# Performance work log

Hardware: AMD Instinct MI355X
Metric: run time of the kernel (lower is better)

Reference implementation:

```python
import jax, jax.numpy as jnp
import numpy as np

WINDOW_SIZE = 11
WINDOW_SIGMA = 1.5
LOSS_WEIGHT = 1.0
PAD = WINDOW_SIZE // 2  # 5; applied to BOTH H and W as in the torch source


def _gaussian_window(channels):
    # Matches torch gaussian_window: 1-D gaussian reshaped to (1,1,1,ws),
    # repeated per channel -> OIHW kernel of shape (C, 1, 1, ws).
    coords = np.arange(WINDOW_SIZE, dtype=np.float32) - (WINDOW_SIZE // 2)
    g = np.exp(-coords ** 2 / (2.0 * WINDOW_SIGMA ** 2))
    g = g / g.sum()
    w = np.tile(g.reshape(1, 1, 1, WINDOW_SIZE), (channels, 1, 1, 1))
    return jnp.asarray(w)


def _dwconv(x, w, channels):
    # Depthwise conv, kernel (1, ws), zero padding 5 on both H and W
    # (faithful to F.conv2d(..., padding=5) with a (1,11) kernel, which
    # grows H by 10 -- intentional reproduction of the source behavior).
    return jax.lax.conv_general_dilated(
        x, w,
        window_strides=(1, 1),
        padding=((PAD, PAD), (PAD, PAD)),
        dimension_numbers=('NCHW', 'OIHW', 'NCHW'),
        feature_group_count=channels,
    )


def setup_inputs() -> dict:
    key = jax.random.key(0)
    k1, k2 = jax.random.split(key)
    shape = (16, 3, 512, 512)
    pred = jax.random.uniform(k1, shape, dtype=jnp.float32)
    target = jax.random.uniform(k2, shape, dtype=jnp.float32)
    return {"pred": pred, "target": target}


def reference(pred, target):
    channels = pred.shape[1]
    w = _gaussian_window(channels)
    conv = lambda x: _dwconv(x, w, channels)

    mu1 = conv(pred)              # (B, C, H+10, W)
    mu2 = conv(target)
    mu1_sq = mu1 * mu1
    mu2_sq = mu2 * mu2
    mu1_mu2 = mu1 * mu2

    sigma1_sq = conv(pred * pred) - mu1_sq
    sigma2_sq = conv(target * target) - mu2_sq
    sigma12 = conv(pred * target) - mu1_mu2

    C1 = 0.01 ** 2
    C2 = 0.03 ** 2
    ssim_map = ((2.0 * mu1_mu2 + C1) * (2.0 * sigma12 + C2)) / (
        (mu1_sq + mu2_sq + C1) * (sigma1_sq + sigma2_sq + C2))

    return LOSS_WEIGHT * (1.0 - ssim_map.mean())
```

## Files before the change

kernel.cpp:

```cpp
#include <hip/hip_runtime.h>
#include <hip/hip_fp16.h>
#include <cmath>

#define WS 11

typedef unsigned int u32x4_t __attribute__((ext_vector_type(4)));

struct GaussHalf {
    unsigned gA[WS];
    unsigned gS[WS];
    unsigned c11, c22;
};

__device__ __forceinline__ u32x4_t make_row_srsrc(const float* p) {
    const unsigned long long a = (unsigned long long)p;
    u32x4_t r;
    r.x = (unsigned)a;
    r.y = (unsigned)(a >> 32);
    r.z = 2048u;
    r.w = 0x00020000u;
    return r;
}
__device__ __forceinline__ float4 bl_x4(u32x4_t srd, int voff) {
    float4 d;
    asm volatile("buffer_load_dwordx4 %0, %1, %2, 0 offen"
                 : "=v"(d) : "v"(voff), "s"(srd));
    return d;
}
__device__ __forceinline__ float bl_x1(u32x4_t srd, int voff) {
    float d;
    asm volatile("buffer_load_dword %0, %1, %2, 0 offen"
                 : "=v"(d) : "v"(voff), "s"(srd));
    return d;
}

__global__ __launch_bounds__(128, 6) void ssim_row_kernel(
    const float* __restrict__ pred, const float* __restrict__ targ,
    GaussHalf gh, float* __restrict__ partials)
{
    const int t = threadIdx.x;
    const int lane = t & 63;
    const int wid = __builtin_amdgcn_readfirstlane((blockIdx.x << 1) | (t >> 6));

    const int l8 = 8 * lane;
    const int vL1 = 4 * (l8 - 5);
    const int vL4 = 4 * (l8 - 4);
    const int vA  = 4 * l8;
    const int vB  = 4 * (l8 + 4);
    const int vR4 = 4 * (l8 + 8);
    const int vR1 = 4 * (l8 + 12);

    const u32x4_t sp = make_row_srsrc(pred + (long long)wid * 512);
    const u32x4_t sq = make_row_srsrc(targ + (long long)wid * 512);

    const float  pL1 = bl_x1(sp, vL1);
    const float4 pL4 = bl_x4(sp, vL4);
    const float4 pA  = bl_x4(sp, vA);
    const float4 pB  = bl_x4(sp, vB);
    const float4 pR4 = bl_x4(sp, vR4);
    const float  pR1 = bl_x1(sp, vR1);
    const float  qL1 = bl_x1(sq, vL1);
    const float4 qL4 = bl_x4(sq, vL4);
    const float4 qA  = bl_x4(sq, vA);
    const float4 qB  = bl_x4(sq, vB);
    const float4 qR4 = bl_x4(sq, vR4);
    const float  qR1 = bl_x1(sq, vR1);
    asm volatile("s_waitcnt vmcnt(0)" ::: "memory");
    __builtin_amdgcn_sched_barrier(0);

    const float pv[18] = {pL1, pL4.x, pL4.y, pL4.z, pL4.w,
                          pA.x, pA.y, pA.z, pA.w, pB.x, pB.y, pB.z, pB.w,
                          pR4.x, pR4.y, pR4.z, pR4.w, pR1};
    const float qv[18] = {qL1, qL4.x, qL4.y, qL4.z, qL4.w,
                          qA.x, qA.y, qA.z, qA.w, qB.x, qB.y, qB.z, qB.w,
                          qR4.x, qR4.y, qR4.z, qR4.w, qR1};

    const __half2 pm = __halves2half2(__float2half(1.f), __float2half(-1.f));
    const __half2 C11 = __builtin_bit_cast(__half2, gh.c11);
    const __half2 C22 = __builtin_bit_cast(__half2, gh.c22);

    __half2 w[18], s[18];
    #pragma unroll
    for (int i = 0; i < 18; ++i) {
        w[i] = __floats2half2_rn(pv[i] + qv[i], pv[i] - qv[i]);
        s[i] = __hmul2(w[i], w[i]);
    }

    float acc = 0.f;
    #pragma unroll
    for (int px = 0; px < 8; ++px) {
        __half2 AB  = __builtin_bit_cast(__half2, 0u);
        __half2 SUV = __builtin_bit_cast(__half2, 0u);
        #pragma unroll
        for (int k = 0; k < WS; ++k) {
            AB  = __hfma2(__builtin_bit_cast(__half2, gh.gA[k]),
                          w[px + k], AB);
            SUV = __hfma2(__builtin_bit_cast(__half2, gh.gS[k]),
                          s[px + k], SUV);
        }
        const __half2 ab2  = __hmul2(AB, AB);
        const __half2 t2d2 = __hfma2(__lowhigh2highlow(ab2), pm, ab2);
        const __half2 tsds = __hfma2(__lowhigh2highlow(SUV), pm, SUV);
        const __half2 dn1  = __hfma2(t2d2, pm, C11);
        const __half2 dl   = __hsub2(tsds, t2d2);
        const __half2 dn2  = __hfma2(dl, pm, C22);
        const __half2 nd   = __hmul2(dn1, dn2);
        const float dd = __half2float(__low2half(nd));
        const float nn = __half2float(__high2half(nd));
        acc = fmaf(nn, __builtin_amdgcn_rcpf(dd), acc);
    }

    #pragma unroll
    for (int offr = 32; offr > 0; offr >>= 1)
        acc += __shfl_down(acc, offr);
    if (lane == 0)
        partials[wid] = acc;
}

__global__ __launch_bounds__(1024) void ssim_final_kernel(
    const float* __restrict__ partials, float* __restrict__ out)
{
    const int t = threadIdx.x;
    double d = 0.0;
    #pragma unroll
    for (int i = 0; i < 24; ++i)
        d += (double)partials[t + 1024 * i];
    #pragma unroll
    for (int offr = 32; offr > 0; offr >>= 1)
        d += __shfl_down(d, offr);
    __shared__ double wsumd[16];
    const int lane = t & 63, wave = t >> 6;
    if (lane == 0) wsumd[wave] = d;
    __syncthreads();
    if (t == 0) {
        double s = 245760.0;
        #pragma unroll
        for (int i = 0; i < 16; ++i) s += wsumd[i];
        out[0] = (float)(1.0 - s / 12828672.0);
    }
}

static unsigned packh2(float x) {
    const __half h = __float2half(x);
    unsigned short hb;
    __builtin_memcpy(&hb, &h, 2);
    return ((unsigned)hb << 16) | hb;
}

extern "C" void kernel_launch(void* const* d_in, const int* in_sizes, int n_in,
                              void* d_out, int out_size, void* d_ws, size_t ws_size,
                              hipStream_t stream) {
    const float* pred = (const float*)d_in[0];
    const float* targ = (const float*)d_in[1];
    float* out = (float*)d_out;
    float* partials = (float*)d_ws;

    GaussHalf gh;
    double graw[WS], s = 0.0;
    for (int i = 0; i < WS; ++i) {
        const double c = (double)(i - WS / 2);
        graw[i] = exp(-c * c / (2.0 * 1.5 * 1.5));
        s += graw[i];
    }
    for (int i = 0; i < WS; ++i) {
        const double g = graw[i] / s;
        gh.gA[i] = packh2((float)(g * 0.70710678118654752));
        gh.gS[i] = packh2((float)(g * 0.5));
    }
    gh.c11 = packh2(0.0001f);
    gh.c22 = packh2(0.0009f);

    ssim_row_kernel<<<12288, 128, 0, stream>>>(pred, targ, gh, partials);
    ssim_final_kernel<<<1, 1024, 0, stream>>>(partials, out);
}
```

Baseline: 26.58 us.

## Process six rows per wave with software-pipelined buffer loads

Each wave now handles six consecutive rows instead of one. Loads for the next row are issued before the current row is computed, with partial vmcnt waits, so memory latency overlaps the half-precision arithmetic. The grid shrinks to 1024 blocks of 256 threads and the final reduction reads 4096 partials instead of 24576. In exchange, each wave holds two rows of loaded data at once, which raises register pressure, and there are fewer waves in flight to hide latency.

```diff
diff --git a/kernel.cpp b/kernel.cpp
--- a/kernel.cpp
+++ b/kernel.cpp
@@ -34,46 +34,51 @@
     return d;
 }
 
-__global__ __launch_bounds__(128, 6) void ssim_row_kernel(
+struct RowRegs {
+    float4 pL4, pA, pB, pR4, qL4, qA, qB, qR4;
+    float  pL1, pR1, qL1, qR1;
+};
+
+__device__ __forceinline__ RowRegs issue_row(
     const float* __restrict__ pred, const float* __restrict__ targ,
-    GaussHalf gh, float* __restrict__ partials)
-{
-    const int t = threadIdx.x;
-    const int lane = t & 63;
-    const int wid = __builtin_amdgcn_readfirstlane((blockIdx.x << 1) | (t >> 6));
-
-    const int l8 = 8 * lane;
-    const int vL1 = 4 * (l8 - 5);
-    const int vL4 = 4 * (l8 - 4);
-    const int vA  = 4 * l8;
-    const int vB  = 4 * (l8 + 4);
-    const int vR4 = 4 * (l8 + 8);
-    const int vR1 = 4 * (l8 + 12);
-
-    const u32x4_t sp = make_row_srsrc(pred + (long long)wid * 512);
-    const u32x4_t sq = make_row_srsrc(targ + (long long)wid * 512);
-
-    const float  pL1 = bl_x1(sp, vL1);
-    const float4 pL4 = bl_x4(sp, vL4);
-    const float4 pA  = bl_x4(sp, vA);
-    const float4 pB  = bl_x4(sp, vB);
-    const float4 pR4 = bl_x4(sp, vR4);
-    const float  pR1 = bl_x1(sp, vR1);
-    const float  qL1 = bl_x1(sq, vL1);
-    const float4 qL4 = bl_x4(sq, vL4);
-    const float4 qA  = bl_x4(sq, vA);
-    const float4 qB  = bl_x4(sq, vB);
-    const float4 qR4 = bl_x4(sq, vR4);
-    const float  qR1 = bl_x1(sq, vR1);
-    asm volatile("s_waitcnt vmcnt(0)" ::: "memory");
-    __builtin_amdgcn_sched_barrier(0);
-
-    const float pv[18] = {pL1, pL4.x, pL4.y, pL4.z, pL4.w,
-                          pA.x, pA.y, pA.z, pA.w, pB.x, pB.y, pB.z, pB.w,
-                          pR4.x, pR4.y, pR4.z, pR4.w, pR1};
-    const float qv[18] = {qL1, qL4.x, qL4.y, qL4.z, qL4.w,
-                          qA.x, qA.y, qA.z, qA.w, qB.x, qB.y, qB.z, qB.w,
-                          qR4.x, qR4.y, qR4.z, qR4.w, qR1};
+    int row, int vL1, int vL4, int vA, int vB, int vR4, int vR1)
+{
+    const u32x4_t sp = make_row_srsrc(pred + (long long)row * 512);
+    const u32x4_t sq = make_row_srsrc(targ + (long long)row * 512);
+    RowRegs R;
+    R.pL1 = bl_x1(sp, vL1);
+    R.pL4 = bl_x4(sp, vL4);
+    R.pA  = bl_x4(sp, vA);
+    R.pB  = bl_x4(sp, vB);
+    R.pR4 = bl_x4(sp, vR4);
+    R.pR1 = bl_x1(sp, vR1);
+    R.qL1 = bl_x1(sq, vL1);
+    R.qL4 = bl_x4(sq, vL4);
+    R.qA  = bl_x4(sq, vA);
+    R.qB  = bl_x4(sq, vB);
+    R.qR4 = bl_x4(sq, vR4);
+    R.qR1 = bl_x1(sq, vR1);
+    return R;
+}
+
+#define VM_WAIT_12() do { \
+    asm volatile("s_waitcnt vmcnt(12)" ::: "memory"); \
+    __builtin_amdgcn_sched_barrier(0); } while (0)
+#define VM_WAIT_0() do { \
+    asm volatile("s_waitcnt vmcnt(0)" ::: "memory"); \
+    __builtin_amdgcn_sched_barrier(0); } while (0)
+
+__device__ __forceinline__ float compute_row(const RowRegs& R,
+                                             const GaussHalf& gh)
+{
+    const float pv[18] = {R.pL1, R.pL4.x, R.pL4.y, R.pL4.z, R.pL4.w,
+                          R.pA.x, R.pA.y, R.pA.z, R.pA.w,
+                          R.pB.x, R.pB.y, R.pB.z, R.pB.w,
+                          R.pR4.x, R.pR4.y, R.pR4.z, R.pR4.w, R.pR1};
+    const float qv[18] = {R.qL1, R.qL4.x, R.qL4.y, R.qL4.z, R.qL4.w,
+                          R.qA.x, R.qA.y, R.qA.z, R.qA.w,
+                          R.qB.x, R.qB.y, R.qB.z, R.qB.w,
+                          R.qR4.x, R.qR4.y, R.qR4.z, R.qR4.w, R.qR1};
 
     const __half2 pm = __halves2half2(__float2half(1.f), __float2half(-1.f));
     const __half2 C11 = __builtin_bit_cast(__half2, gh.c11);
@@ -109,6 +114,50 @@
         const float nn = __half2float(__high2half(nd));
         acc = fmaf(nn, __builtin_amdgcn_rcpf(dd), acc);
     }
+    return acc;
+}
+
+__global__ __launch_bounds__(256, 4) void ssim_row_kernel(
+    const float* __restrict__ pred, const float* __restrict__ targ,
+    GaussHalf gh, float* __restrict__ partials)
+{
+    const int t = threadIdx.x;
+    const int lane = t & 63;
+    const int wid = __builtin_amdgcn_readfirstlane((blockIdx.x << 2) | (t >> 6));
+    const int row0 = wid * 6;
+
+    const int l8 = 8 * lane;
+    const int vL1 = 4 * (l8 - 5);
+    const int vL4 = 4 * (l8 - 4);
+    const int vA  = 4 * l8;
+    const int vB  = 4 * (l8 + 4);
+    const int vR4 = 4 * (l8 + 8);
+    const int vR1 = 4 * (l8 + 12);
+
+    RowRegs R0 = issue_row(pred, targ, row0 + 0, vL1, vL4, vA, vB, vR4, vR1);
+    RowRegs R1 = issue_row(pred, targ, row0 + 1, vL1, vL4, vA, vB, vR4, vR1);
+
+    VM_WAIT_12();
+    RowRegs R2 = issue_row(pred, targ, row0 + 2, vL1, vL4, vA, vB, vR4, vR1);
+    float acc = compute_row(R0, gh);
+
+    VM_WAIT_12();
+    RowRegs R3 = issue_row(pred, targ, row0 + 3, vL1, vL4, vA, vB, vR4, vR1);
+    acc += compute_row(R1, gh);
+
+    VM_WAIT_12();
+    RowRegs R4 = issue_row(pred, targ, row0 + 4, vL1, vL4, vA, vB, vR4, vR1);
+    acc += compute_row(R2, gh);
+
+    VM_WAIT_12();
+    RowRegs R5 = issue_row(pred, targ, row0 + 5, vL1, vL4, vA, vB, vR4, vR1);
+    acc += compute_row(R3, gh);
+
+    VM_WAIT_12();
+    acc += compute_row(R4, gh);
+
+    VM_WAIT_0();
+    acc += compute_row(R5, gh);
 
     #pragma unroll
     for (int offr = 32; offr > 0; offr >>= 1)
@@ -123,7 +172,7 @@
     const int t = threadIdx.x;
     double d = 0.0;
     #pragma unroll
-    for (int i = 0; i < 24; ++i)
+    for (int i = 0; i < 4; ++i)
         d += (double)partials[t + 1024 * i];
     #pragma unroll
     for (int offr = 32; offr > 0; offr >>= 1)
@@ -170,6 +219,6 @@
     gh.c11 = packh2(0.0001f);
     gh.c22 = packh2(0.0009f);
 
-    ssim_row_kernel<<<12288, 128, 0, stream>>>(pred, targ, gh, partials);
+    ssim_row_kernel<<<1024, 256, 0, stream>>>(pred, targ, gh, partials);
     ssim_final_kernel<<<1, 1024, 0, stream>>>(partials, out);
 }
```

After: 27.03 us. No clear change (+1.7%).
